# Optimization experiments

Hardware: AMD Instinct MI355X
Metric: run time of the kernel (lower is better)

Reference implementation:

```python
import jax, jax.numpy as jnp
import numpy as np

DELTA = 6.0      # 3 / (1 - alpha), alpha = 0.5
ETA = 1.0
MS_ITER = 3
D_FEAT = 256
N_PTS = 8192
X_SCALE = 0.06   # keeps ||x||^2 ~ 0.9 so exp(DELTA * X^T X) is well-conditioned


def setup_inputs() -> dict:
    key = jax.random.key(0)
    X = jax.random.normal(key, (D_FEAT, N_PTS), dtype=jnp.float32) * X_SCALE
    return {"X": X}


def _mean_shift_once(X):
    # X: [d, N]
    S = jnp.einsum('dn,dm->nm', X, X)          # X^T X, [N, N]
    K = jnp.exp(DELTA * S)                     # Gaussian-like affinity, [N, N]
    colsum = jnp.sum(K, axis=0)                # d = K^T @ ones  -> column sums, [N]
    # X @ P with P = (1-eta) I + eta K D_inv; D_inv = diag(1/colsum).
    # X @ K @ D_inv == (X @ K) / colsum (per-column scaling) -- no diag/eye materialized.
    XK = X @ K                                 # [d, N]
    return (1.0 - ETA) * X + ETA * (XK / colsum[None, :])


def reference(X):
    outs = []
    cur = X
    for _ in range(MS_ITER):
        cur = _mean_shift_once(cur)
        outs.append(cur)
    return tuple(outs)
```

## Files before the change

### kernel.cpp

```cpp
#include <hip/hip_runtime.h>
#include <hip/hip_bf16.h>
#include <stdint.h>

#define DFEAT 256
#define NPTS  8192

typedef __attribute__((ext_vector_type(8)))  short bf16x8;
typedef __attribute__((ext_vector_type(16))) float f32x16;
typedef __attribute__((ext_vector_type(4)))  int   int4v;
typedef __attribute__((ext_vector_type(4)))  float f32x4;

#define AS1 __attribute__((address_space(1)))
#define AS3 __attribute__((address_space(3)))

__device__ inline void dma16(const void* g, void* l) {
  __builtin_amdgcn_global_load_lds((const AS1 uint32_t*)g, (AS3 uint32_t*)l, 16, 0, 0);
}

__device__ inline uint16_t f2bf(float f) {
  union { float f; uint32_t u; } v; v.f = f;
  return (uint16_t)((v.u + 0x7FFFu + ((v.u >> 16) & 1u)) >> 16);
}


__global__ __launch_bounds__(256, 2) void ms_fused(
    const uint16_t* __restrict__ xaf,
    const uint16_t* __restrict__ xbf,
    float* __restrict__ nump,
    float* __restrict__ csp)
{
  __shared__ __attribute__((aligned(16))) uint16_t XT[2][16384];
  __shared__ __attribute__((aligned(16))) uint16_t Ps[2][4096];

  const int tid  = threadIdx.x;
  const int w    = tid >> 6;
  const int lane = tid & 63;
  const int l31  = lane & 31;
  const int g    = lane >> 5;
  const int bid  = blockIdx.x;
  const int mt   = (bid & 1) | ((bid >> 3) << 1);
  const int q    = (bid >> 1) & 3;
  const int m0   = mt * 64;
  const int a_sub = w >> 1;
  const int b_sub = w & 1;

  const char* xafc = (const char*)xaf;
  const char* xbfc = (const char*)xbf;
  char*       XTc  = (char*)XT;
  char*       Psc  = (char*)Ps;

  bf16x8 Bm[16];
  {
    const char* bp = xafc + (size_t)(m0 / 32 + b_sub) * 16384 + g * 512 + l31 * 16;
    #pragma unroll
    for (int ks = 0; ks < 16; ++ks)
      Bm[ks] = __builtin_bit_cast(bf16x8, *(const int4v*)(bp + ks * 1024));
  }

  f32x16 accO[2][2];
  #pragma unroll
  for (int i = 0; i < 2; ++i)
    #pragma unroll
    for (int j = 0; j < 2; ++j)
      #pragma unroll
      for (int r = 0; r < 16; ++r) accO[i][j][r] = 0.0f;
  float csacc = 0.0f;

  const int mloc = 32 * b_sub + l31;
  const int l7   = l31 & 7;
  const int j0   = q * 32;

  {
    const char* src = xafc + (size_t)j0 * 32768;
    #pragma unroll
    for (int r = 0; r < 8; ++r)
      dma16(src + tid * 16 + r * 4096, XTc + tid * 16 + r * 4096);
  }
  __syncthreads();

  bf16x8 XfE[2][4], XfO[2][4];

#define MS_BODY(T_, CUR_, XF_LD, XF_USE, DO_PV)                               \
  {                                                                           \
    const int jt_ = j0 + (T_);                                                \
    char*       psW_ = Psc + (CUR_) * 8192;                                   \
    const char* psR_ = Psc + ((CUR_) ^ 1) * 8192;                             \
                         \
    if ((T_) < 31) {                                                          \
      const char* src_ = xafc + (size_t)(jt_ + 1) * 32768;                    \
      _Pragma("unroll")                                                       \
      for (int r = 0; r < 8; ++r)                                             \
        dma16(src_ + tid * 16 + r * 4096,                                     \
              XTc + ((CUR_) ^ 1) * 32768 + tid * 16 + r * 4096);              \
    }                                                                         \
                                \
    {                                                                         \
      const int n0_ = jt_ * 64;                                               \
      _Pragma("unroll")                                                       \
      for (int t2 = 0; t2 < 2; ++t2) {                                        \
        const char* xp_ = xbfc + (size_t)(2 * w + t2) * 524288 +              \
                          (size_t)(n0_ >> 3) * 512 + g * 512 + l31 * 16;      \
        _Pragma("unroll")                                                     \
        for (int ks = 0; ks < 4; ++ks)                                        \
          XF_LD[t2][ks] =                                                     \
              __builtin_bit_cast(bf16x8, *(const int4v*)(xp_ + ks * 1024));   \
      }                                                                       \
    }                                                                         \
              \
    __builtin_amdgcn_sched_barrier(0x38F);                                    \
              \
    f32x16 s;                                                                 \
    _Pragma("unroll")                                                         \
    for (int r = 0; r < 16; ++r) s[r] = 0.0f;                                 \
    {                                                                         \
      const char* ap_ = XTc + (CUR_) * 32768 + a_sub * 16384 + g * 512 +      \
                        l31 * 16;                                             \
      _Pragma("unroll")                                                       \
      for (int ks = 0; ks < 16; ++ks) {                                       \
        bf16x8 A = __builtin_bit_cast(bf16x8,                                 \
                                      *(const int4v*)(ap_ + ks * 1024));      \
        s = __builtin_amdgcn_mfma_f32_32x32x16_bf16(A, Bm[ks], s, 0, 0, 0);   \
      }                                                                       \
    }                                                                         \
                                \
    if (DO_PV) {                                                              \
      _Pragma("unroll")                                                       \
      for (int ks = 0; ks < 4; ++ks) {                                        \
        bf16x8 Bp[2];                                                         \
        _Pragma("unroll")                                                     \
        for (int mm = 0; mm < 2; ++mm) {                                      \
          int mrow = 32 * mm + l31;                                           \
          int p = (2 * ks + g) ^ l7;                                          \
          Bp[mm] = __builtin_bit_cast(bf16x8,                                 \
              *(const int4v*)(psR_ + mrow * 128 + p * 16));                   \
        }                                                                     \
        _Pragma("unroll")                                                     \
        for (int t2 = 0; t2 < 2; ++t2) {                                      \
          accO[t2][0] = __builtin_amdgcn_mfma_f32_32x32x16_bf16(              \
              XF_USE[t2][ks], Bp[0], accO[t2][0], 0, 0, 0);                   \
          accO[t2][1] = __builtin_amdgcn_mfma_f32_32x32x16_bf16(              \
              XF_USE[t2][ks], Bp[1], accO[t2][1], 0, 0, 0);                   \
        }                                                                     \
      }                                                                       \
    }                                                                         \
                        \
    _Pragma("unroll")                                                         \
    for (int k = 0; k < 4; ++k) {                                             \
      float e0 = __expf(6.0f * s[4 * k + 0]);                                 \
      float e1 = __expf(6.0f * s[4 * k + 1]);                                 \
      float e2 = __expf(6.0f * s[4 * k + 2]);                                 \
      float e3 = __expf(6.0f * s[4 * k + 3]);                                 \
      csacc += (e0 + e1) + (e2 + e3);                                         \
      uint32_t lo, hi;                                                        \
      asm("v_cvt_pk_bf16_f32 %0, %1, %2" : "=v"(lo) : "v"(e0), "v"(e1));      \
      asm("v_cvt_pk_bf16_f32 %0, %1, %2" : "=v"(hi) : "v"(e2), "v"(e3));      \
      int p = (4 * a_sub + k) ^ (mloc & 7);                                   \
      *(uint64_t*)(psW_ + mloc * 128 + p * 16 + 8 * g) =                      \
          ((uint64_t)hi << 32) | lo;                                          \
    }                                                                         \
          \
    asm volatile("s_waitcnt vmcnt(8) lgkmcnt(0)" ::: "memory");               \
    __builtin_amdgcn_s_barrier();                                             \
  }

  MS_BODY(0, 0, XfE, XfO, false)
  for (int tp = 0; tp < 15; ++tp) {
    const int tb = 2 * tp;
    MS_BODY(tb + 1, 1, XfO, XfE, true)
    MS_BODY(tb + 2, 0, XfE, XfO, true)
  }
  MS_BODY(31, 1, XfO, XfE, true)
#undef MS_BODY

  {
    const char* psR = Psc + 8192;
    #pragma unroll
    for (int ks = 0; ks < 4; ++ks) {
      bf16x8 Bp[2];
      #pragma unroll
      for (int mm = 0; mm < 2; ++mm) {
        int mrow = 32 * mm + l31;
        int p = (2 * ks + g) ^ l7;
        Bp[mm] = __builtin_bit_cast(bf16x8,
            *(const int4v*)(psR + mrow * 128 + p * 16));
      }
      #pragma unroll
      for (int t2 = 0; t2 < 2; ++t2) {
        accO[t2][0] = __builtin_amdgcn_mfma_f32_32x32x16_bf16(XfO[t2][ks], Bp[0], accO[t2][0], 0,0,0);
        accO[t2][1] = __builtin_amdgcn_mfma_f32_32x32x16_bf16(XfO[t2][ks], Bp[1], accO[t2][1], 0,0,0);
      }
    }
  }

  csacc += __shfl_xor(csacc, 32, 64);
  if (g == 0) csp[(size_t)(2 * q + a_sub) * NPTS + m0 + mloc] = csacc;
  float* np = nump + (size_t)q * (DFEAT * (size_t)NPTS);
  #pragma unroll
  for (int t2 = 0; t2 < 2; ++t2)
    #pragma unroll
    for (int mm = 0; mm < 2; ++mm)
      #pragma unroll
      for (int r = 0; r < 16; ++r) {
        int drow = 32 * (2 * w + t2) + (r & 3) + 8 * (r >> 2) + 4 * g;
        int mg   = m0 + 32 * mm + l31;
        np[(size_t)drow * NPTS + mg] = accO[t2][mm][r];
      }
}

__global__ __launch_bounds__(256) void ms_combine(
    const float* __restrict__ src, const float* __restrict__ csp,
    float* __restrict__ yout,
    uint16_t* __restrict__ xaf, uint16_t* __restrict__ xbf,
    const int mode)
{
  __shared__ uint16_t T[64][66];
  const int tid = threadIdx.x;
  const int n0 = blockIdx.x * 64;
  const int d0 = blockIdx.y * 64;

  f32x4 rinv;
  if (mode) {
    const int nq = tid & 15;
    f32x4 c = *(const f32x4*)(csp + n0 + nq * 4);
    #pragma unroll
    for (int s2 = 1; s2 < 8; ++s2)
      c += *(const f32x4*)(csp + (size_t)s2 * NPTS + n0 + nq * 4);
    rinv[0] = 1.0f / c[0]; rinv[1] = 1.0f / c[1];
    rinv[2] = 1.0f / c[2]; rinv[3] = 1.0f / c[3];
  }

  #pragma unroll
  for (int i = 0; i < 4; ++i) {
    int e  = tid + i * 256;
    int dl = e >> 4, nq = e & 15;
    size_t idx = (size_t)(d0 + dl) * NPTS + (n0 + nq * 4);
    f32x4 v = *(const f32x4*)(src + idx);
    if (mode) {
      v += *(const f32x4*)(src + idx + (size_t)1 * DFEAT * NPTS);
      v += *(const f32x4*)(src + idx + (size_t)2 * DFEAT * NPTS);
      v += *(const f32x4*)(src + idx + (size_t)3 * DFEAT * NPTS);
      v *= rinv;
      *(f32x4*)(yout + idx) = v;
    }
    #pragma unroll
    for (int k = 0; k < 4; ++k) T[dl][nq * 4 + k] = f2bf(v[k]);
  }
  __syncthreads();

  char* xafc = (char*)xaf;
  char* xbfc = (char*)xbf;
  #pragma unroll
  for (int i = 0; i < 2; ++i) {
    int c  = tid + i * 256;
    int nb = c >> 8, s2 = (c >> 5) & 7, ln = c & 31;
    union { uint32_t u[4]; int4v v; } pk;
    #pragma unroll
    for (int k = 0; k < 4; ++k) {
      uint32_t lo = T[s2 * 8 + 2 * k][nb * 32 + ln];
      uint32_t hi = T[s2 * 8 + 2 * k + 1][nb * 32 + ln];
      pk.u[k] = lo | (hi << 16);
    }
    *(int4v*)(xafc + (size_t)(n0 / 32 + nb) * 16384 +
              (size_t)(d0 / 8 + s2) * 512 + ln * 16) = pk.v;
  }
  #pragma unroll
  for (int i = 0; i < 2; ++i) {
    int c  = tid + i * 256;
    int db = c >> 8, uu = (c >> 5) & 7, ln = c & 31;
    const uint16_t* tr = &T[db * 32 + ln][uu * 8];
    union { uint32_t u[4]; int4v v; } pk;
    #pragma unroll
    for (int k = 0; k < 4; ++k)
      pk.u[k] = (uint32_t)tr[2 * k] | ((uint32_t)tr[2 * k + 1] << 16);
    *(int4v*)(xbfc + (size_t)(d0 / 32 + db) * 524288 +
              (size_t)(n0 / 8 + uu) * 512 + ln * 16) = pk.v;
  }
}

extern "C" void kernel_launch(void* const* d_in, const int* in_sizes, int n_in,
                              void* d_out, int out_size, void* d_ws, size_t ws_size,
                              hipStream_t stream)
{
  (void)in_sizes; (void)n_in; (void)out_size; (void)ws_size;
  const float* X = (const float*)d_in[0];
  float* out = (float*)d_out;
  char* ws = (char*)d_ws;
  uint16_t* xaf  = (uint16_t*)(ws);
  uint16_t* xbf  = (uint16_t*)(ws + (4u << 20));
  float*    nump = (float*)   (ws + (8u << 20));
  float*    csp  = (float*)   (ws + (40u << 20));


  dim3 cgrid(NPTS / 64, DFEAT / 64);
  ms_combine<<<cgrid, 256, 0, stream>>>(X, nullptr, nullptr, xaf, xbf, 0);
  for (int it = 0; it < 3; ++it) {
    ms_fused<<<512, 256, 0, stream>>>(xaf, xbf, nump, csp);
    ms_combine<<<cgrid, 256, 0, stream>>>(nump, csp,
                                          out + (size_t)it * DFEAT * NPTS,
                                          xaf, xbf, 1);
  }
}
```

Baseline: 303.3 us.

## Fuse combine step into main kernel via last-block ticket and double-buffered operands

```diff
diff --git a/kernel.cpp b/kernel.cpp
--- a/kernel.cpp
+++ b/kernel.cpp
@@ -22,12 +22,16 @@
   return (uint16_t)((v.u + 0x7FFFu + ((v.u >> 16) & 1u)) >> 16);
 }
 
-
 __global__ __launch_bounds__(256, 2) void ms_fused(
-    const uint16_t* __restrict__ xaf,
-    const uint16_t* __restrict__ xbf,
+    const uint16_t* __restrict__ xafr,
+    const uint16_t* __restrict__ xbfr,
+    uint16_t* __restrict__ xafw,
+    uint16_t* __restrict__ xbfw,
     float* __restrict__ nump,
-    float* __restrict__ csp)
+    float* __restrict__ csp,
+    int*   __restrict__ ticket,
+    float* __restrict__ yout,
+    const int it, const int last)
 {
   __shared__ __attribute__((aligned(16))) uint16_t XT[2][16384];
   __shared__ __attribute__((aligned(16))) uint16_t Ps[2][4096];
@@ -44,8 +48,8 @@
   const int a_sub = w >> 1;
   const int b_sub = w & 1;
 
-  const char* xafc = (const char*)xaf;
-  const char* xbfc = (const char*)xbf;
+  const char* xafc = (const char*)xafr;
+  const char* xbfc = (const char*)xbfr;
   char*       XTc  = (char*)XT;
   char*       Psc  = (char*)Ps;
 
@@ -194,40 +198,100 @@
 
   csacc += __shfl_xor(csacc, 32, 64);
   if (g == 0) csp[(size_t)(2 * q + a_sub) * NPTS + m0 + mloc] = csacc;
-  float* np = nump + (size_t)q * (DFEAT * (size_t)NPTS);
-  #pragma unroll
-  for (int t2 = 0; t2 < 2; ++t2)
-    #pragma unroll
-    for (int mm = 0; mm < 2; ++mm)
-      #pragma unroll
-      for (int r = 0; r < 16; ++r) {
-        int drow = 32 * (2 * w + t2) + (r & 3) + 8 * (r >> 2) + 4 * g;
-        int mg   = m0 + 32 * mm + l31;
-        np[(size_t)drow * NPTS + mg] = accO[t2][mm][r];
+  {
+    float* np = nump + (size_t)q * (DFEAT * (size_t)NPTS);
+    #pragma unroll
+    for (int t2 = 0; t2 < 2; ++t2)
+      #pragma unroll
+      for (int mm = 0; mm < 2; ++mm)
+        #pragma unroll
+        for (int r = 0; r < 16; ++r) {
+          int drow = 32 * (2 * w + t2) + (r & 3) + 8 * (r >> 2) + 4 * g;
+          int mg   = m0 + 32 * mm + l31;
+          np[(size_t)drow * NPTS + mg] = accO[t2][mm][r];
+        }
+  }
+
+  __threadfence();
+  if (tid == 0) {
+    int old = atomicAdd(&ticket[mt], 1);
+    *(int*)Psc = (old == 4 * it + 3) ? 1 : 0;
+  }
+  __syncthreads();
+  if (*(const int*)Psc == 0) return;
+  __threadfence();
+
+  float* csl = (float*)(Psc + 64);
+  if (tid < 64) {
+    float c = 0.0f;
+    #pragma unroll
+    for (int s2 = 0; s2 < 8; ++s2)
+      c += csp[(size_t)s2 * NPTS + m0 + tid];
+    csl[tid] = 1.0f / c;
+  }
+  uint16_t (*T)[66] = (uint16_t (*)[66])XTc;
+
+  for (int d0 = 0; d0 < 256; d0 += 64) {
+    __syncthreads();
+    #pragma unroll
+    for (int i = 0; i < 4; ++i) {
+      int e  = tid + i * 256;
+      int dl = e >> 4, mq = e & 15;
+      size_t idx = (size_t)(d0 + dl) * NPTS + m0 + mq * 4;
+      f32x4 v = *(const f32x4*)(nump + idx);
+      v += *(const f32x4*)(nump + idx + (size_t)1 * DFEAT * NPTS);
+      v += *(const f32x4*)(nump + idx + (size_t)2 * DFEAT * NPTS);
+      v += *(const f32x4*)(nump + idx + (size_t)3 * DFEAT * NPTS);
+      v *= *((const f32x4*)csl + mq);
+      *(f32x4*)(yout + idx) = v;
+      #pragma unroll
+      for (int k = 0; k < 4; ++k) T[dl][mq * 4 + k] = f2bf(v[k]);
+    }
+    __syncthreads();
+    if (!last) {
+      char* xafo = (char*)xafw;
+      char* xbfo = (char*)xbfw;
+      #pragma unroll
+      for (int i = 0; i < 2; ++i) {
+        int c  = tid + i * 256;
+        int nb = c >> 8, s2 = (c >> 5) & 7, ln = c & 31;
+        union { uint32_t u[4]; int4v v; } pk;
+        #pragma unroll
+        for (int k = 0; k < 4; ++k) {
+          uint32_t lo = T[s2 * 8 + 2 * k][nb * 32 + ln];
+          uint32_t hi = T[s2 * 8 + 2 * k + 1][nb * 32 + ln];
+          pk.u[k] = lo | (hi << 16);
+        }
+        *(int4v*)(xafo + (size_t)(m0 / 32 + nb) * 16384 +
+                  (size_t)(d0 / 8 + s2) * 512 + ln * 16) = pk.v;
       }
-}
-
-__global__ __launch_bounds__(256) void ms_combine(
-    const float* __restrict__ src, const float* __restrict__ csp,
-    float* __restrict__ yout,
+      #pragma unroll
+      for (int i = 0; i < 2; ++i) {
+        int c  = tid + i * 256;
+        int db = c >> 8, uu = (c >> 5) & 7, ln = c & 31;
+        const uint16_t* tr = &T[db * 32 + ln][uu * 8];
+        union { uint32_t u[4]; int4v v; } pk;
+        #pragma unroll
+        for (int k = 0; k < 4; ++k)
+          pk.u[k] = (uint32_t)tr[2 * k] | ((uint32_t)tr[2 * k + 1] << 16);
+        *(int4v*)(xbfo + (size_t)(d0 / 32 + db) * 524288 +
+                  (size_t)(m0 / 8 + uu) * 512 + ln * 16) = pk.v;
+      }
+    }
+  }
+}
+
+__global__ __launch_bounds__(256) void ms_init(
+    const float* __restrict__ src,
     uint16_t* __restrict__ xaf, uint16_t* __restrict__ xbf,
-    const int mode)
+    int* __restrict__ ticket)
 {
   __shared__ uint16_t T[64][66];
   const int tid = threadIdx.x;
   const int n0 = blockIdx.x * 64;
   const int d0 = blockIdx.y * 64;
 
-  f32x4 rinv;
-  if (mode) {
-    const int nq = tid & 15;
-    f32x4 c = *(const f32x4*)(csp + n0 + nq * 4);
-    #pragma unroll
-    for (int s2 = 1; s2 < 8; ++s2)
-      c += *(const f32x4*)(csp + (size_t)s2 * NPTS + n0 + nq * 4);
-    rinv[0] = 1.0f / c[0]; rinv[1] = 1.0f / c[1];
-    rinv[2] = 1.0f / c[2]; rinv[3] = 1.0f / c[3];
-  }
+  if (blockIdx.x == 0 && blockIdx.y == 0 && tid < 128) ticket[tid] = 0;
 
   #pragma unroll
   for (int i = 0; i < 4; ++i) {
@@ -235,13 +299,6 @@
     int dl = e >> 4, nq = e & 15;
     size_t idx = (size_t)(d0 + dl) * NPTS + (n0 + nq * 4);
     f32x4 v = *(const f32x4*)(src + idx);
-    if (mode) {
-      v += *(const f32x4*)(src + idx + (size_t)1 * DFEAT * NPTS);
-      v += *(const f32x4*)(src + idx + (size_t)2 * DFEAT * NPTS);
-      v += *(const f32x4*)(src + idx + (size_t)3 * DFEAT * NPTS);
-      v *= rinv;
-      *(f32x4*)(yout + idx) = v;
-    }
     #pragma unroll
     for (int k = 0; k < 4; ++k) T[dl][nq * 4 + k] = f2bf(v[k]);
   }
@@ -285,18 +342,21 @@
   const float* X = (const float*)d_in[0];
   float* out = (float*)d_out;
   char* ws = (char*)d_ws;
-  uint16_t* xaf  = (uint16_t*)(ws);
-  uint16_t* xbf  = (uint16_t*)(ws + (4u << 20));
-  float*    nump = (float*)   (ws + (8u << 20));
-  float*    csp  = (float*)   (ws + (40u << 20));
-
+  uint16_t* xaf0 = (uint16_t*)(ws);
+  uint16_t* xbf0 = (uint16_t*)(ws + (4u  << 20));
+  uint16_t* xaf1 = (uint16_t*)(ws + (8u  << 20));
+  uint16_t* xbf1 = (uint16_t*)(ws + (12u << 20));
+  float*    nump = (float*)   (ws + (16u << 20));
+  float*    csp  = (float*)   (ws + (48u << 20));
+  int*      tick = (int*)     (ws + (48u << 20) + (1u << 18));
 
   dim3 cgrid(NPTS / 64, DFEAT / 64);
-  ms_combine<<<cgrid, 256, 0, stream>>>(X, nullptr, nullptr, xaf, xbf, 0);
-  for (int it = 0; it < 3; ++it) {
-    ms_fused<<<512, 256, 0, stream>>>(xaf, xbf, nump, csp);
-    ms_combine<<<cgrid, 256, 0, stream>>>(nump, csp,
-                                          out + (size_t)it * DFEAT * NPTS,
-                                          xaf, xbf, 1);
-  }
-}
+  ms_init<<<cgrid, 256, 0, stream>>>(X, xaf0, xbf0, tick);
+  const size_t OS = (size_t)DFEAT * NPTS;
+  ms_fused<<<512, 256, 0, stream>>>(xaf0, xbf0, xaf1, xbf1, nump, csp, tick,
+                                    out + 0 * OS, 0, 0);
+  ms_fused<<<512, 256, 0, stream>>>(xaf1, xbf1, xaf0, xbf0, nump, csp, tick,
+                                    out + 1 * OS, 1, 0);
+  ms_fused<<<512, 256, 0, stream>>>(xaf0, xbf0, xaf1, xbf1, nump, csp, tick,
+                                    out + 2 * OS, 2, 1);
+}
```

Result: slower. 560.1 us (+84.7%).
